# Kernel tuning notes

Hardware: AMD Instinct MI355X
Metric: run time of the kernel (lower is better)

The kernel has to match this reference:

```python
import jax, jax.numpy as jnp
import numpy as np

NPOINT, NSAMPLE, RADIUS, EPS = 128, 32, 0.4, 1e-5
C_IN, C_MID, C_OUT = 256, 256, 256


def setup_inputs() -> dict:
    key = jax.random.key(0)
    ks = jax.random.split(key, 6)
    B, N = 8, 16384
    xyz = jax.random.uniform(ks[0], (B, N, 3), dtype=jnp.float32)
    feats = jax.random.normal(ks[1], (B, N, C_IN), dtype=jnp.float32)
    # SharedMLP: Conv2d 1x1 (no bias, followed by BN) layers 259->256, 256->256
    w1 = jax.random.normal(ks[2], (C_MID, C_IN + 3), dtype=jnp.float32) * 0.05
    w2 = jax.random.normal(ks[3], (C_OUT, C_MID), dtype=jnp.float32) * 0.05
    gamma1 = jnp.ones((C_MID,), jnp.float32); beta1 = jnp.zeros((C_MID,), jnp.float32)
    mean1 = jnp.zeros((C_MID,), jnp.float32); var1 = jnp.ones((C_MID,), jnp.float32)
    gamma2 = jnp.ones((C_OUT,), jnp.float32); beta2 = jnp.zeros((C_OUT,), jnp.float32)
    mean2 = jnp.zeros((C_OUT,), jnp.float32); var2 = jnp.ones((C_OUT,), jnp.float32)
    return {"xyz": xyz, "proposal_features": feats,
            "w1": w1, "gamma1": gamma1, "beta1": beta1, "mean1": mean1, "var1": var1,
            "w2": w2, "gamma2": gamma2, "beta2": beta2, "mean2": mean2, "var2": var2}


def fps(xyz, npoint):
    # Farthest point sampling, CUDA-kernel-faithful: starts at index 0.
    B, N, _ = xyz.shape
    def step(carry, _):
        dist, far = carry
        centroid = jnp.take_along_axis(xyz, far[:, None, None], axis=1)  # [B,1,3]
        d = jnp.sum((xyz - centroid) ** 2, axis=-1)                      # [B,N]
        dist = jnp.minimum(dist, d)
        return (dist, jnp.argmax(dist, axis=-1).astype(jnp.int32)), far
    init = (jnp.full((B, N), 1e10, xyz.dtype), jnp.zeros((B,), jnp.int32))
    _, inds = jax.lax.scan(step, init, None, length=npoint)
    return inds.T  # [B, npoint]


def ball_query(xyz, new_xyz, radius, nsample):
    # First-nsample-in-order points within radius, padded with the first hit.
    B, N, _ = xyz.shape
    d2 = jnp.sum((new_xyz[:, :, None, :] - xyz[:, None, :, :]) ** 2, axis=-1)  # [B,S,N]
    keys = jnp.where(d2 < radius * radius, jnp.arange(N, dtype=jnp.int32), N)
    idx = -jax.lax.top_k(-keys, nsample)[0]  # smallest indices, ascending
    idx = jnp.where(idx < N, idx, idx[..., :1])  # pad invalid with first hit
    return jnp.clip(idx, 0, N - 1)


def gather_points(pts_bnc, idx):
    # pts_bnc [B,N,C], idx [B,S,K] -> [B,S,K,C]
    B, S, K = idx.shape
    flat = jnp.take_along_axis(pts_bnc, idx.reshape(B, S * K)[:, :, None], axis=1)
    return flat.reshape(B, S, K, pts_bnc.shape[-1])


def bn_relu(x, gamma, beta, mean, var):
    return jax.nn.relu((x - mean) * jax.lax.rsqrt(var + EPS) * gamma + beta)


def reference(xyz, proposal_features, w1, gamma1, beta1, mean1, var1,
              w2, gamma2, beta2, mean2, var2):
    # proposal_features arrives as [B, N, C]; torch module permutes to [B, C, N]
    # (we keep channels-last internally, equivalent math).
    inds = fps(xyz, NPOINT)                                   # [B,128]
    new_xyz = jnp.take_along_axis(xyz, inds[:, :, None], axis=1)  # [B,128,3]
    idx = ball_query(xyz, new_xyz, RADIUS, NSAMPLE)           # [B,128,32]
    g_xyz = gather_points(xyz, idx) - new_xyz[:, :, None, :]  # [B,128,32,3]
    g_feat = gather_points(proposal_features, idx)            # [B,128,32,256]
    x = jnp.concatenate([g_xyz, g_feat], axis=-1)             # [B,128,32,259]
    h = bn_relu(jnp.einsum('bskc,oc->bsko', x, w1), gamma1, beta1, mean1, var1)
    h = bn_relu(jnp.einsum('bskc,oc->bsko', h, w2), gamma2, beta2, mean2, var2)
    new_features = jnp.max(h, axis=2)                         # [B,128,256]
    return jnp.transpose(new_features, (0, 2, 1))             # [B,256,128]
```

## Files before the change

### kernel.cpp

```cpp
#include <hip/hip_runtime.h>
#include <hip/hip_bf16.h>
#include <cstdint>
#include <cstddef>

#define NB      8
#define NPTS    16384
#define NPOINT  128
#define NSAMPLE 32
#define CIN     256
#define CMID    256
#define COUT    256
#define KDIM    259
#define KPAD    288
#define XS_STRIDE 296
#define HS_STRIDE 264

typedef __attribute__((ext_vector_type(8))) short bf16x8;
typedef __attribute__((ext_vector_type(4))) float f32x4;

__device__ __forceinline__ short f2bf(float f) {
  unsigned u = __float_as_uint(f);
  u += 0x7fffu + ((u >> 16) & 1u);
  return (short)(u >> 16);
}

#define FPS_T 1024
#define FPS_W (FPS_T / 64)
#define FPS_P (NPTS / FPS_T)
#define DIST_STRIDE 20

__global__ __launch_bounds__(FPS_T) __attribute__((amdgpu_waves_per_eu(4, 4)))
void fps_kernel(const float* __restrict__ xyz, int* __restrict__ inds) {
  const int b = blockIdx.x;
  const int t = threadIdx.x;
  const int lane = t & 63, w = t >> 6;
  const float* xb = xyz + (size_t)b * NPTS * 3;

  float c[48];
  {
    const float4* src = (const float4*)(xb + (size_t)t * FPS_P * 3);
#pragma unroll
    for (int q = 0; q < 12; ++q) {
      float4 v = src[q];
      c[q * 4 + 0] = v.x; c[q * 4 + 1] = v.y; c[q * 4 + 2] = v.z; c[q * 4 + 3] = v.w;
    }
  }
#pragma unroll
  for (int q = 0; q < 48; q += 3)
    asm volatile("" : "+v"(c[q]), "+v"(c[q + 1]), "+v"(c[q + 2]));

  __shared__ float sdist[FPS_T * DIST_STRIDE];
  float4* dvec = (float4*)(sdist + t * DIST_STRIDE);
#pragma unroll
  for (int q = 0; q < 4; ++q) dvec[q] = make_float4(1e10f, 1e10f, 1e10f, 1e10f);

  __shared__ unsigned long long s_pack[2][FPS_W];
  __shared__ float swx[2][FPS_W], swy[2][FPS_W], swz[2][FPS_W];

  int far = 0;
  float cx = xb[0], cy = xb[1], cz = xb[2];

  for (int it = 0; it < NPOINT; ++it) {
    if (t == 0) inds[b * NPOINT + it] = far;
    float best = -1.0f;
    int bi = 0;
#pragma unroll
    for (int q = 0; q < 4; ++q) {
      float4 dv = dvec[q];
      float dm[4];
#pragma unroll
      for (int r = 0; r < 4; ++r) {
        const int i = q * 4 + r;
        float dx = __fsub_rn(c[3 * i + 0], cx);
        float dy = __fsub_rn(c[3 * i + 1], cy);
        float dz = __fsub_rn(c[3 * i + 2], cz);
        float d  = __fadd_rn(__fadd_rn(__fmul_rn(dx, dx), __fmul_rn(dy, dy)), __fmul_rn(dz, dz));
        dm[r] = fminf((&dv.x)[r], d);
      }
#pragma unroll
      for (int r = 0; r < 4; ++r) {
        if (dm[r] > best) { best = dm[r]; bi = t * FPS_P + q * 4 + r; }
      }
      dvec[q] = make_float4(dm[0], dm[1], dm[2], dm[3]);
    }
#pragma unroll
    for (int off = 32; off > 0; off >>= 1) {
      float ov = __shfl_down(best, off, 64);
      int   oi = __shfl_down(bi, off, 64);
      if (ov > best || (ov == best && oi < bi)) { best = ov; bi = oi; }
    }
    const int par = it & 1;
    if (lane == 0) {
      s_pack[par][w] = ((unsigned long long)__float_as_uint(best) << 18)
                     | ((unsigned long long)(unsigned)(NPTS - 1 - bi) << 4)
                     | (unsigned long long)w;
      swx[par][w] = xb[bi * 3 + 0];
      swy[par][w] = xb[bi * 3 + 1];
      swz[par][w] = xb[bi * 3 + 2];
    }
    __syncthreads();
    unsigned long long pm = s_pack[par][lane & 15];
#pragma unroll
    for (int off = 8; off > 0; off >>= 1) {
      unsigned long long o = __shfl_xor(pm, off, 64);
      if (o > pm) pm = o;
    }
    const int wi = (int)(pm & 15ull);
    far = (NPTS - 1) - (int)((pm >> 4) & (unsigned long long)(NPTS - 1));
    cx = swx[par][wi]; cy = swy[par][wi]; cz = swz[par][wi];
  }
}

__global__ __launch_bounds__(256) void ballq_kernel(const float* __restrict__ xyz,
                                                    const int* __restrict__ inds,
                                                    int* __restrict__ idx) {
  const int gw   = (blockIdx.x * 256 + threadIdx.x) >> 6;
  const int lane = threadIdx.x & 63;
  const int b = gw >> 7, s = gw & 127;
  const float* xb = xyz + (size_t)b * NPTS * 3;
  const int ind = inds[b * NPOINT + s];
  const float cx = xb[ind * 3 + 0], cy = xb[ind * 3 + 1], cz = xb[ind * 3 + 2];
  int* o = idx + gw * NSAMPLE;
  const float R2 = (float)(0.4 * 0.4);
  int total = 0;
  int first_hit = 0;
  bool have_first = false;
  for (int base = 0; base < NPTS && total < NSAMPLE; base += 64) {
    const int j = base + lane;
    float dx = __fsub_rn(xb[j * 3 + 0], cx);
    float dy = __fsub_rn(xb[j * 3 + 1], cy);
    float dz = __fsub_rn(xb[j * 3 + 2], cz);
    float d2 = __fadd_rn(__fadd_rn(__fmul_rn(dx, dx), __fmul_rn(dy, dy)), __fmul_rn(dz, dz));
    bool hit = d2 < R2;
    unsigned long long m = __ballot(hit);
    if (!have_first && m) { first_hit = base + (int)__builtin_ctzll(m); have_first = true; }
    int pos = total + (int)__popcll(m & ((1ull << lane) - 1ull));
    if (hit && pos < NSAMPLE) o[pos] = j;
    total += (int)__popcll(m);
  }
  for (int p = total + lane; p < NSAMPLE; p += 64) o[p] = first_hit;
}

__global__ __launch_bounds__(256) void prep_kernel(
    const float* __restrict__ w1, const float* __restrict__ g1, const float* __restrict__ be1,
    const float* __restrict__ m1, const float* __restrict__ v1,
    const float* __restrict__ w2, const float* __restrict__ g2, const float* __restrict__ be2,
    const float* __restrict__ m2, const float* __restrict__ v2,
    short* __restrict__ w1b, short* __restrict__ w2b,
    float* __restrict__ b1, float* __restrict__ b2) {
  int i = blockIdx.x * 256 + threadIdx.x;
  if (i < CMID * KPAD) {
    int oc = i / KPAD, c = i - oc * KPAD;
    float a = g1[oc] * rsqrtf(v1[oc] + 1e-5f);
    float val = (c < KDIM) ? w1[oc * KDIM + c] * a : 0.0f;
    w1b[i] = f2bf(val);
    if (c == 0) b1[oc] = be1[oc] - m1[oc] * a;
  }
  if (i < COUT * CMID) {
    int oc = i >> 8, c = i & 255;
    float a = g2[oc] * rsqrtf(v2[oc] + 1e-5f);
    w2b[i] = f2bf(w2[oc * CMID + c] * a);
    if (c == 0) b2[oc] = be2[oc] - m2[oc] * a;
  }
}

__global__ __launch_bounds__(256) void mlp_kernel(
    const float* __restrict__ xyz, const float* __restrict__ feats,
    const int* __restrict__ inds, const int* __restrict__ idx,
    const short* __restrict__ w1b, const short* __restrict__ w2b,
    const float* __restrict__ b1, const float* __restrict__ b2,
    float* __restrict__ out) {
  const int g   = blockIdx.x;
  const int bb  = g >> 7, s = g & 127;
  const int tid = threadIdx.x;
  const int wave = tid >> 6, lane = tid & 63;
  const int lrow = lane & 15, quad = lane >> 4;

  __shared__ short Xs[32 * XS_STRIDE];
  __shared__ short Hs[32 * HS_STRIDE];
  __shared__ int   sj[NSAMPLE];
  __shared__ float scen[3];

  if (tid < NSAMPLE) sj[tid] = idx[g * NSAMPLE + tid];
  if (tid < 3) {
    int ind = inds[bb * NPOINT + s];
    scen[tid] = xyz[((size_t)bb * NPTS + ind) * 3 + tid];
  }
  __syncthreads();

  for (int e = tid; e < 32 * KPAD; e += 256) {
    int r = e / KPAD, c = e - r * KPAD;
    int j = sj[r];
    float val;
    if (c < 3)          val = xyz[((size_t)bb * NPTS + j) * 3 + c] - scen[c];
    else if (c < KDIM)  val = feats[((size_t)bb * NPTS + j) * CIN + (c - 3)];
    else                val = 0.0f;
    Xs[r * XS_STRIDE + c] = f2bf(val);
  }
  __syncthreads();

  const int nw = wave * 64;
  f32x4 acc[4][2];
#pragma unroll
  for (int nt = 0; nt < 4; ++nt)
#pragma unroll
    for (int mt = 0; mt < 2; ++mt) acc[nt][mt] = (f32x4){0.f, 0.f, 0.f, 0.f};

  for (int ks = 0; ks < 9; ++ks) {
    const int ko = ks * 32 + quad * 8;
    bf16x8 a0 = *(const bf16x8*)(&Xs[lrow * XS_STRIDE + ko]);
    bf16x8 a1 = *(const bf16x8*)(&Xs[(lrow + 16) * XS_STRIDE + ko]);
#pragma unroll
    for (int nt = 0; nt < 4; ++nt) {
      const int oc = nw + nt * 16 + lrow;
      bf16x8 bf = *(const bf16x8*)(w1b + oc * KPAD + ko);
      acc[nt][0] = __builtin_amdgcn_mfma_f32_16x16x32_bf16(a0, bf, acc[nt][0], 0, 0, 0);
      acc[nt][1] = __builtin_amdgcn_mfma_f32_16x16x32_bf16(a1, bf, acc[nt][1], 0, 0, 0);
    }
  }

#pragma unroll
  for (int nt = 0; nt < 4; ++nt) {
    const int oc = nw + nt * 16 + lrow;
    const float bias = b1[oc];
#pragma unroll
    for (int mt = 0; mt < 2; ++mt) {
#pragma unroll
      for (int r = 0; r < 4; ++r) {
        int row = mt * 16 + quad * 4 + r;
        float h = fmaxf(acc[nt][mt][r] + bias, 0.0f);
        Hs[row * HS_STRIDE + oc] = f2bf(h);
      }
    }
  }
  __syncthreads();

#pragma unroll
  for (int nt = 0; nt < 4; ++nt)
#pragma unroll
    for (int mt = 0; mt < 2; ++mt) acc[nt][mt] = (f32x4){0.f, 0.f, 0.f, 0.f};

  for (int ks = 0; ks < 8; ++ks) {
    const int ko = ks * 32 + quad * 8;
    bf16x8 a0 = *(const bf16x8*)(&Hs[lrow * HS_STRIDE + ko]);
    bf16x8 a1 = *(const bf16x8*)(&Hs[(lrow + 16) * HS_STRIDE + ko]);
#pragma unroll
    for (int nt = 0; nt < 4; ++nt) {
      const int oc = nw + nt * 16 + lrow;
      bf16x8 bf = *(const bf16x8*)(w2b + oc * CMID + ko);
      acc[nt][0] = __builtin_amdgcn_mfma_f32_16x16x32_bf16(a0, bf, acc[nt][0], 0, 0, 0);
      acc[nt][1] = __builtin_amdgcn_mfma_f32_16x16x32_bf16(a1, bf, acc[nt][1], 0, 0, 0);
    }
  }

#pragma unroll
  for (int nt = 0; nt < 4; ++nt) {
    const int oc = nw + nt * 16 + lrow;
    const float bias = b2[oc];
    float v = -3.4e38f;
#pragma unroll
    for (int mt = 0; mt < 2; ++mt) {
      f32x4 a = acc[nt][mt];
      v = fmaxf(v, fmaxf(fmaxf(a[0], a[1]), fmaxf(a[2], a[3])));
    }
    v = fmaxf(v + bias, 0.0f);
    v = fmaxf(v, __shfl_xor(v, 16, 64));
    v = fmaxf(v, __shfl_xor(v, 32, 64));
    if (lane < 16) out[((size_t)bb * COUT + oc) * NPOINT + s] = v;
  }
}

extern "C" void kernel_launch(void* const* d_in, const int* in_sizes, int n_in,
                              void* d_out, int out_size, void* d_ws, size_t ws_size,
                              hipStream_t stream) {
  const float* xyz   = (const float*)d_in[0];
  const float* feats = (const float*)d_in[1];
  const float* w1    = (const float*)d_in[2];
  const float* g1    = (const float*)d_in[3];
  const float* be1   = (const float*)d_in[4];
  const float* m1    = (const float*)d_in[5];
  const float* v1    = (const float*)d_in[6];
  const float* w2    = (const float*)d_in[7];
  const float* g2    = (const float*)d_in[8];
  const float* be2   = (const float*)d_in[9];
  const float* m2    = (const float*)d_in[10];
  const float* v2    = (const float*)d_in[11];
  float* out = (float*)d_out;

  char* ws = (char*)d_ws;
  int*   inds = (int*)(ws);
  int*   idx  = (int*)(ws + 4096);
  short* w1b  = (short*)(ws + 135168);
  short* w2b  = (short*)(ws + 282624);
  float* b1   = (float*)(ws + 413696);
  float* b2   = (float*)(ws + 414720);

  prep_kernel<<<288, 256, 0, stream>>>(w1, g1, be1, m1, v1, w2, g2, be2, m2, v2,
                                       w1b, w2b, b1, b2);
  fps_kernel<<<NB, FPS_T, 0, stream>>>(xyz, inds);
  ballq_kernel<<<256, 256, 0, stream>>>(xyz, inds, idx);
  mlp_kernel<<<NB * NPOINT, 256, 0, stream>>>(xyz, feats, inds, idx, w1b, w2b, b1, b2, out);
}
```

Baseline: 518.4 us.

## Split FPS point storage between LDS and registers with interleaved distances

The FPS kernel used to keep 16 points per thread in registers with their running distances in LDS. Now half the points (8 per thread) live in LDS as xyz+dist float4s, and the other half (from the upper half of the array) sit in registers along with their distances. This lowers register pressure and the number of LDS distance round trips, but adds LDS coordinate loads every iteration and a 36-float per-thread LDS stride. The tie-break order changes because indices are no longer contiguous per thread. It is unclear whether the first-index tie-break is preserved.

```diff
diff --git a/kernel.cpp b/kernel.cpp
--- a/kernel.cpp
+++ b/kernel.cpp
@@ -26,8 +26,7 @@
 
 #define FPS_T 1024
 #define FPS_W (FPS_T / 64)
-#define FPS_P (NPTS / FPS_T)
-#define DIST_STRIDE 20
+#define PT_STRIDE 36
 
 __global__ __launch_bounds__(FPS_T) __attribute__((amdgpu_waves_per_eu(4, 4)))
 void fps_kernel(const float* __restrict__ xyz, int* __restrict__ inds) {
@@ -36,26 +35,41 @@
   const int lane = t & 63, w = t >> 6;
   const float* xb = xyz + (size_t)b * NPTS * 3;
 
-  float c[48];
-  {
-    const float4* src = (const float4*)(xb + (size_t)t * FPS_P * 3);
-#pragma unroll
-    for (int q = 0; q < 12; ++q) {
-      float4 v = src[q];
-      c[q * 4 + 0] = v.x; c[q * 4 + 1] = v.y; c[q * 4 + 2] = v.z; c[q * 4 + 3] = v.w;
-    }
-  }
-#pragma unroll
-  for (int q = 0; q < 48; q += 3)
-    asm volatile("" : "+v"(c[q]), "+v"(c[q + 1]), "+v"(c[q + 2]));
-
-  __shared__ float sdist[FPS_T * DIST_STRIDE];
-  float4* dvec = (float4*)(sdist + t * DIST_STRIDE);
-#pragma unroll
-  for (int q = 0; q < 4; ++q) dvec[q] = make_float4(1e10f, 1e10f, 1e10f, 1e10f);
-
+  __shared__ float spts[FPS_T * PT_STRIDE];
   __shared__ unsigned long long s_pack[2][FPS_W];
   __shared__ float swx[2][FPS_W], swy[2][FPS_W], swz[2][FPS_W];
+
+  float4* lpt = (float4*)(spts + t * PT_STRIDE);
+  {
+    const float4* s4 = (const float4*)(xb + (size_t)t * 8 * 3);
+    float v[24];
+#pragma unroll
+    for (int q = 0; q < 6; ++q) {
+      float4 x = s4[q];
+      v[4 * q + 0] = x.x; v[4 * q + 1] = x.y; v[4 * q + 2] = x.z; v[4 * q + 3] = x.w;
+    }
+#pragma unroll
+    for (int p = 0; p < 8; ++p)
+      lpt[p] = make_float4(v[3 * p + 0], v[3 * p + 1], v[3 * p + 2], 1e10f);
+  }
+  float rx[8], ry[8], rz[8], rdist[8];
+  {
+    const float4* s4 = (const float4*)(xb + (size_t)(8192 + t * 8) * 3);
+    float v[24];
+#pragma unroll
+    for (int q = 0; q < 6; ++q) {
+      float4 x = s4[q];
+      v[4 * q + 0] = x.x; v[4 * q + 1] = x.y; v[4 * q + 2] = x.z; v[4 * q + 3] = x.w;
+    }
+#pragma unroll
+    for (int p = 0; p < 8; ++p) {
+      rx[p] = v[3 * p + 0]; ry[p] = v[3 * p + 1]; rz[p] = v[3 * p + 2];
+      rdist[p] = 1e10f;
+    }
+  }
+#pragma unroll
+  for (int p = 0; p < 8; ++p)
+    asm volatile("" : "+v"(rx[p]), "+v"(ry[p]), "+v"(rz[p]));
 
   int far = 0;
   float cx = xb[0], cy = xb[1], cz = xb[2];
@@ -65,23 +79,25 @@
     float best = -1.0f;
     int bi = 0;
 #pragma unroll
-    for (int q = 0; q < 4; ++q) {
-      float4 dv = dvec[q];
-      float dm[4];
-#pragma unroll
-      for (int r = 0; r < 4; ++r) {
-        const int i = q * 4 + r;
-        float dx = __fsub_rn(c[3 * i + 0], cx);
-        float dy = __fsub_rn(c[3 * i + 1], cy);
-        float dz = __fsub_rn(c[3 * i + 2], cz);
-        float d  = __fadd_rn(__fadd_rn(__fmul_rn(dx, dx), __fmul_rn(dy, dy)), __fmul_rn(dz, dz));
-        dm[r] = fminf((&dv.x)[r], d);
-      }
-#pragma unroll
-      for (int r = 0; r < 4; ++r) {
-        if (dm[r] > best) { best = dm[r]; bi = t * FPS_P + q * 4 + r; }
-      }
-      dvec[q] = make_float4(dm[0], dm[1], dm[2], dm[3]);
+    for (int p = 0; p < 8; ++p) {
+      float4 v = lpt[p];
+      float dx = __fsub_rn(v.x, cx);
+      float dy = __fsub_rn(v.y, cy);
+      float dz = __fsub_rn(v.z, cz);
+      float d  = __fadd_rn(__fadd_rn(__fmul_rn(dx, dx), __fmul_rn(dy, dy)), __fmul_rn(dz, dz));
+      float dm = fminf(v.w, d);
+      ((float*)(lpt + p))[3] = dm;
+      if (dm > best) { best = dm; bi = t * 8 + p; }
+    }
+#pragma unroll
+    for (int p = 0; p < 8; ++p) {
+      float dx = __fsub_rn(rx[p], cx);
+      float dy = __fsub_rn(ry[p], cy);
+      float dz = __fsub_rn(rz[p], cz);
+      float d  = __fadd_rn(__fadd_rn(__fmul_rn(dx, dx), __fmul_rn(dy, dy)), __fmul_rn(dz, dz));
+      float dm = fminf(rdist[p], d);
+      rdist[p] = dm;
+      if (dm > best) { best = dm; bi = 8192 + t * 8 + p; }
     }
 #pragma unroll
     for (int off = 32; off > 0; off >>= 1) {
```

Measured after the change: 547.7 us. 5.7% more time.
